# Kernel tuning notes

Hardware: AMD Instinct MI355X
Metric: run time of the kernel (lower is better)

Reference implementation:

```python
import jax, jax.numpy as jnp
import numpy as np

DEPTH = 2
DIM = 512
HEADS = 8
DH = 64
INNER = HEADS * DH
MLP = 2048
B = 2
N = 2048
EPS = 1e-6
NEG = -float(np.finfo(np.float32).max)
SCALE = DH ** -0.5


def setup_inputs() -> dict:
    key = jax.random.key(0)
    ks = jax.random.split(key, 8)
    inp = {
        'x': jax.random.normal(ks[0], (B, N, DIM), dtype=jnp.float32),
        'mask': jax.random.randint(ks[1], (B, N), 0, 2, dtype=jnp.int32),
        'qkv_w': 0.02 * jax.random.normal(ks[2], (DEPTH, DIM, 3 * INNER), dtype=jnp.float32),
        'out_w': 0.02 * jax.random.normal(ks[3], (DEPTH, INNER, DIM), dtype=jnp.float32),
        'out_b': jnp.zeros((DEPTH, DIM), dtype=jnp.float32),
        'ff_w1': 0.02 * jax.random.normal(ks[4], (DEPTH, DIM, MLP), dtype=jnp.float32),
        'ff_b1': jnp.zeros((DEPTH, MLP), dtype=jnp.float32),
        'ff_w2': 0.02 * jax.random.normal(ks[5], (DEPTH, MLP, DIM), dtype=jnp.float32),
        'ff_b2': jnp.zeros((DEPTH, DIM), dtype=jnp.float32),
        'ad1_w': jnp.ones((DEPTH, B * DIM), dtype=jnp.float32),
        'ad1_b': jnp.zeros((DEPTH, B * DIM), dtype=jnp.float32),
        'ad2_w': jnp.ones((DEPTH, B * DIM), dtype=jnp.float32),
        'ad2_b': jnp.zeros((DEPTH, B * DIM), dtype=jnp.float32),
    }
    return inp


def adain(x, w, b):
    # AdaptiveInstanceNorm2d: batch_norm over channels (B*D), spatial dim N, training=True
    # -> per-(b, d) mean/biased-var over N, affine params of shape (B*D,) -> (B,1,D)
    mu = jnp.mean(x, axis=1, keepdims=True)
    var = jnp.var(x, axis=1, keepdims=True)  # biased variance, as in batch_norm
    xn = (x - mu) * jax.lax.rsqrt(var + EPS)
    b_sz, _, d = x.shape
    return xn * w.reshape(b_sz, 1, d) + b.reshape(b_sz, 1, d)


def attention(x, mask2d, qkv_w, out_w, out_b):
    b_sz, n, _ = x.shape
    qkv = x @ qkv_w  # [B,N,3*INNER]
    q, k, v = jnp.split(qkv, 3, axis=-1)

    def split_heads(t):
        return t.reshape(b_sz, n, HEADS, DH).transpose(0, 2, 1, 3)  # [B,H,N,D]

    q, k, v = split_heads(q), split_heads(k), split_heads(v)
    dots = jnp.einsum('bhnd,bhmd->bhnm', q, k) * SCALE  # [B,H,N,N]
    dots = jnp.where(mask2d[:, None] == 0, NEG, dots)
    attn = jax.nn.softmax(dots, axis=-1)
    out = jnp.einsum('bhnm,bhmd->bhnd', attn, v)
    out = out.transpose(0, 2, 1, 3).reshape(b_sz, n, INNER)
    return out @ out_w + out_b


def feedforward(x, w1, b1, w2, b2):
    h = jax.nn.gelu(x @ w1 + b1, approximate=False)  # torch nn.GELU default = exact erf
    return h @ w2 + b2


def reference(x, mask, qkv_w, out_w, out_b, ff_w1, ff_b1, ff_w2, ff_b2,
              ad1_w, ad1_b, ad2_w, ad2_b):
    mask2d = mask[:, :, None] * mask[:, None, :]  # [B,N,N]
    for l in range(DEPTH):
        h = adain(x, ad1_w[l], ad1_b[l])
        x = attention(h, mask2d, qkv_w[l], out_w[l], out_b[l]) + x
        h = adain(x, ad2_w[l], ad2_b[l])
        x = feedforward(h, ff_w1[l], ff_b1[l], ff_w2[l], ff_b2[l]) + x
    return x
```

## Files before the change

### kernel.cpp

```cpp
#include <hip/hip_runtime.h>
#include <hip/hip_bf16.h>

#define DEPTHL 2
#define DIMM   512
#define NHEADS 8
#define DHH    64
#define INNERD 512
#define MLPD   2048
#define BB     2
#define SEQL   2048
#define ROWS   (BB*SEQL)
#define MNEG   (-1.0e38f)
#define SCLQ   0.18033688f
#define NSPLIT 4
#define KPS    (SEQL / NSPLIT)

typedef __attribute__((ext_vector_type(4))) float f32x4;
typedef __attribute__((ext_vector_type(8))) __bf16 bf16x8;

#define GLDS16(g, l) __builtin_amdgcn_global_load_lds((const __attribute__((address_space(1))) void*)(g), (__attribute__((address_space(3))) void*)(l), 16, 0, 0)

__device__ __forceinline__ unsigned short f2bf(float f) {
  union { float f; unsigned int u; } v; v.f = f;
  unsigned int r = v.u + 0x7fffu + ((v.u >> 16) & 1u);
  return (unsigned short)(r >> 16);
}
__device__ __forceinline__ float bf2f(unsigned short h) {
  union { unsigned int u; float f; } v; v.u = ((unsigned int)h) << 16; return v.f;
}
__device__ __forceinline__ unsigned int cvtpk(float a, float b) {
  unsigned int r;
  asm("v_cvt_pk_bf16_f32 %0, %1, %2" : "=v"(r) : "v"(a), "v"(b));
  return r;
}

__global__ __launch_bounds__(256) void wtrans(const float* __restrict__ wsrc,
                                              unsigned short* __restrict__ wdst,
                                              int K, int N) {
  __shared__ float t[32][33];
  const float* src = wsrc + (size_t)blockIdx.z * K * N;
  unsigned short* dst = wdst + (size_t)blockIdx.z * K * N;
  int k0 = blockIdx.x * 32, n0 = blockIdx.y * 32;
  int tx = threadIdx.x & 31, ty = threadIdx.x >> 5;
#pragma unroll
  for (int j = 0; j < 32; j += 8)
    t[ty + j][tx] = src[(size_t)(k0 + ty + j) * N + n0 + tx];
  __syncthreads();
#pragma unroll
  for (int j = 0; j < 32; j += 8)
    dst[(size_t)(n0 + ty + j) * K + k0 + tx] = f2bf(t[tx][ty + j]);
}

__global__ __launch_bounds__(512) void adain_p1(const float* __restrict__ x,
                                                float* __restrict__ p1, float* __restrict__ p2) {
  int d = threadIdx.x, c = blockIdx.x, b = blockIdx.y;
  const float* xp = x + ((size_t)b * SEQL + c * 64) * DIMM + d;
  float s = 0.f, s2 = 0.f;
  for (int i = 0; i < 64; ++i) { float v = xp[(size_t)i * DIMM]; s += v; s2 += v * v; }
  p1[(b * 32 + c) * DIMM + d] = s;
  p2[(b * 32 + c) * DIMM + d] = s2;
}

__global__ __launch_bounds__(512) void adain_p2(const float* __restrict__ p1, const float* __restrict__ p2,
                                                const float* __restrict__ w, const float* __restrict__ bi,
                                                float* __restrict__ alpha, float* __restrict__ beta) {
  int d = threadIdx.x, b = blockIdx.x;
  float s = 0.f, s2 = 0.f;
  for (int c = 0; c < 32; ++c) { s += p1[(b * 32 + c) * DIMM + d]; s2 += p2[(b * 32 + c) * DIMM + d]; }
  float mean = s * (1.0f / SEQL);
  float var = s2 * (1.0f / SEQL) - mean * mean;
  float a = w[b * DIMM + d] * rsqrtf(var + 1e-6f);
  alpha[b * DIMM + d] = a;
  beta[b * DIMM + d] = bi[b * DIMM + d] - mean * a;
}

__global__ __launch_bounds__(256) void adain_apply(const float* __restrict__ x,
                                                   const float* __restrict__ alpha, const float* __restrict__ beta,
                                                   unsigned short* __restrict__ hb) {
  int idx = blockIdx.x * 256 + threadIdx.x;
  int d = idx & (DIMM - 1);
  int b = idx >> 20;
  hb[idx] = f2bf(x[idx] * alpha[b * DIMM + d] + beta[b * DIMM + d]);
}

__global__ __launch_bounds__(256) void maskbuild(const int* __restrict__ mask, float* __restrict__ maskadd) {
  int i = blockIdx.x * 256 + threadIdx.x;
  maskadd[i] = mask[i] ? 0.f : MNEG;
}

template <int EPI, int BN>
__global__ __launch_bounds__(256)
void gemm_k(const unsigned short* __restrict__ A,
            const unsigned short* __restrict__ Wt,
            const float* __restrict__ bias,
            const float* __restrict__ resid,
            float* __restrict__ outF,
            unsigned short* __restrict__ outB,
            unsigned short* __restrict__ part,
            int N, int Kt) {
  constexpr int NI = BN / 32;
  __shared__ __align__(16) unsigned short As[2][128 * 32];
  __shared__ __align__(16) unsigned short Bs[2][BN * 32];
  const int tid = threadIdx.x;
  const int w = tid >> 6, lane = tid & 63;

  unsigned int f = blockIdx.y * gridDim.x + blockIdx.x;
  unsigned int grp = f & 7u, idx = f >> 3;
  unsigned int rpx = gridDim.y >> 3;
  unsigned int by = grp * rpx + idx / gridDim.x;
  unsigned int bx = idx % gridDim.x;

  const int bm = by * 128, bn = bx * BN;
  const int wm = (w >> 1) * 64, wn = (w & 1) * (BN / 2);

  const int nsplit = gridDim.z, sp = blockIdx.z;
  const int Kc = Kt / nsplit;
  const int kbeg = sp * Kc, kend = kbeg + Kc;

  f32x4 acc[4][NI] = {};

  auto stage = [&](int buf, int k0) {
#pragma unroll
    for (int j = 0; j < 2; ++j) {
      int r = w * 32 + (lane >> 2) + j * 16;
      int cl = (lane & 3) ^ ((r >> 1) & 3);
      GLDS16(A + (size_t)(bm + r) * Kt + k0 + cl * 8, &As[buf][(w * 32 + j * 16) * 32]);
    }
    if (BN == 128) {
#pragma unroll
      for (int j = 0; j < 2; ++j) {
        int r = w * 32 + (lane >> 2) + j * 16;
        int cl = (lane & 3) ^ ((r >> 1) & 3);
        GLDS16(Wt + (size_t)(bn + r) * Kt + k0 + cl * 8, &Bs[buf][(w * 32 + j * 16) * 32]);
      }
    } else {
      int r = w * 16 + (lane >> 2);
      int cl = (lane & 3) ^ ((r >> 1) & 3);
      GLDS16(Wt + (size_t)(bn + r) * Kt + k0 + cl * 8, &Bs[buf][(w * 16) * 32]);
    }
  };

  stage(0, kbeg);
  __syncthreads();
  int cur = 0;

  for (int k0 = kbeg; k0 < kend; k0 += 32) {
    if (k0 + 32 < kend) stage(cur ^ 1, k0 + 32);
    bf16x8 af[4], bfr[NI];
#pragma unroll
    for (int i = 0; i < 4; ++i) {
      int ar = wm + i * 16 + (lane & 15);
      int ac = (lane >> 4) ^ ((ar >> 1) & 3);
      af[i] = *(const bf16x8*)&As[cur][ar * 32 + ac * 8];
    }
#pragma unroll
    for (int i = 0; i < NI; ++i) {
      int br = wn + i * 16 + (lane & 15);
      int bc = (lane >> 4) ^ ((br >> 1) & 3);
      bfr[i] = *(const bf16x8*)&Bs[cur][br * 32 + bc * 8];
    }
#pragma unroll
    for (int mi = 0; mi < 4; ++mi)
#pragma unroll
      for (int ni = 0; ni < NI; ++ni)
        acc[mi][ni] = __builtin_amdgcn_mfma_f32_16x16x32_bf16(af[mi], bfr[ni], acc[mi][ni], 0, 0, 0);
    __syncthreads();
    cur ^= 1;
  }

  const size_t MN = (size_t)gridDim.y * 128 * N;
#pragma unroll
  for (int mi = 0; mi < 4; ++mi) {
#pragma unroll
    for (int ni = 0; ni < NI; ++ni) {
#pragma unroll
      for (int r = 0; r < 4; ++r) {
        int row = bm + wm + mi * 16 + (lane >> 4) * 4 + r;
        int col = bn + wn + ni * 16 + (lane & 15);
        float v = acc[mi][ni][r];
        size_t o = (size_t)row * N + col;
        if (EPI == 3) {
          part[(size_t)sp * MN + o] = f2bf(v);
        } else {
          if (bias) v += bias[col];
          if (EPI == 1) v = 0.5f * v * (1.0f + erff(v * 0.70710678118f));
          if (EPI == 2) outF[o] = v + resid[o];
          else if (EPI != 2) outB[o] = f2bf(v);
        }
      }
    }
  }
}

template <int NS>
__global__ __launch_bounds__(256) void comb_k(const unsigned short* __restrict__ part,
                                              const float* __restrict__ bias,
                                              const float* __restrict__ resid,
                                              float* __restrict__ outF) {
  size_t idx = ((size_t)blockIdx.x * 256 + threadIdx.x) * 4;
  int col = (int)(idx & 511);
  float a0 = 0.f, a1 = 0.f, a2 = 0.f, a3 = 0.f;
#pragma unroll
  for (int s = 0; s < NS; ++s) {
    uint2 v = *(const uint2*)&part[(size_t)s * ROWS * 512 + idx];
    a0 += bf2f(v.x & 0xffff); a1 += bf2f(v.x >> 16);
    a2 += bf2f(v.y & 0xffff); a3 += bf2f(v.y >> 16);
  }
  f32x4 b = *(const f32x4*)&bias[col];
  f32x4 rs = *(const f32x4*)&resid[idx];
  f32x4 o;
  o[0] = a0 + b[0] + rs[0]; o[1] = a1 + b[1] + rs[1];
  o[2] = a2 + b[2] + rs[2]; o[3] = a3 + b[3] + rs[3];
  *(f32x4*)&outF[idx] = o;
}

__global__ __launch_bounds__(256) void repack_qk(const unsigned short* __restrict__ qkv,
                                                 unsigned short* __restrict__ q,
                                                 unsigned short* __restrict__ k) {
  int idx = blockIdx.x * 256 + threadIdx.x;
  int d = idx & (INNERD - 1);
  int n = (idx >> 9) & (SEQL - 1);
  int b = idx >> 20;
  int h = d >> 6, dh = d & 63;
  size_t src = (size_t)(b * SEQL + n) * 1536 + d;
  size_t dst = ((size_t)(b * NHEADS + h) * SEQL + n) * DHH + dh;
  q[dst] = f2bf(bf2f(qkv[src]) * SCLQ);
  k[dst] = qkv[src + INNERD];
}

__global__ __launch_bounds__(256) void transpose_v(const unsigned short* __restrict__ qkv,
                                                   unsigned short* __restrict__ vt) {
  __shared__ unsigned short t[64][65];
  int bh = blockIdx.x;
  int nt = blockIdx.y;
  int b = bh >> 3, h = bh & 7;
  for (int i = threadIdx.x; i < 64 * 64; i += 256) {
    int n = i >> 6, dh = i & 63;
    t[n][dh] = qkv[(size_t)(b * SEQL + nt * 64 + n) * 1536 + 2 * INNERD + h * 64 + dh];
  }
  __syncthreads();
  for (int i = threadIdx.x; i < 64 * 64; i += 256) {
    int dh = i >> 6, n = i & 63;
    vt[((size_t)bh * DHH + dh) * SEQL + nt * 64 + n] = t[n][dh];
  }
}

__global__ __launch_bounds__(256) void vmean_k(const unsigned short* __restrict__ vt,
                                               float* __restrict__ vmean) {
  __shared__ float red[256];
  int bh = blockIdx.x, t = threadIdx.x;
  int d = blockIdx.y * 8 + (t >> 5), seg = t & 31;
  const unsigned short* p = vt + ((size_t)bh * 64 + d) * SEQL + seg * 64;
  float s = 0.f;
#pragma unroll
  for (int i = 0; i < 16; ++i) {
    uint2 v = *(const uint2*)&p[i * 4];
    s += bf2f(v.x & 0xffff) + bf2f(v.x >> 16) + bf2f(v.y & 0xffff) + bf2f(v.y >> 16);
  }
  red[t] = s;
  __syncthreads();
  if (t < 8) {
    float a = 0.f;
#pragma unroll
    for (int i = 0; i < 32; ++i) a += red[t * 32 + i];
    vmean[bh * 64 + blockIdx.y * 8 + t] = a * (1.0f / SEQL);
  }
}

__global__ __launch_bounds__(256, 4)
void attn_split(const unsigned short* __restrict__ qg,
                const unsigned short* __restrict__ kg,
                const unsigned short* __restrict__ vtg,
                const float* __restrict__ maskadd,
                unsigned short* __restrict__ opart,
                float* __restrict__ lpart) {
  __shared__ __align__(16) unsigned short Ks[64 * 64];
  __shared__ __align__(16) unsigned short Vts[64 * 64];
  __shared__ __align__(16) unsigned short Ps[4 * 16 * 64];
  const int tid = threadIdx.x, w = tid >> 6, lane = tid & 63;
  const int g = lane >> 4, c = lane & 15;
  const int bh = blockIdx.y, b = bh >> 3;
  const int qt = blockIdx.x;
  const int split = blockIdx.z;
  const int kv0 = split * KPS;
  const int q0 = qt * 64 + w * 16;
  const float* maskb = maskadd + b * SEQL;

  bf16x8 qf[2];
#pragma unroll
  for (int kb = 0; kb < 2; ++kb)
    qf[kb] = *(const bf16x8*)&qg[((size_t)bh * SEQL + q0 + c) * DHH + kb * 32 + g * 8];

  const __bf16 one1 = (__bf16)1.0f;
  const bf16x8 ones = {one1, one1, one1, one1, one1, one1, one1, one1};

  f32x4 o[4] = {};
  f32x4 lones = {};
  unsigned short* myP = &Ps[w * 1024];

  for (int kt = 0; kt < KPS / 64; ++kt) {
#pragma unroll
    for (int j = 0; j < 2; ++j) {
      int r = w * 16 + j * 8 + (lane >> 3);
      int cl = (lane & 7) ^ (r & 7);
      GLDS16(kg + ((size_t)bh * SEQL + kv0 + kt * 64 + r) * DHH + cl * 8, &Ks[(w * 16 + j * 8) * 64]);
      GLDS16(vtg + ((size_t)bh * DHH + r) * SEQL + kv0 + kt * 64 + cl * 8, &Vts[(w * 16 + j * 8) * 64]);
    }
    __syncthreads();

    f32x4 sT[4];
#pragma unroll
    for (int nt = 0; nt < 4; ++nt)
      sT[nt] = *(const f32x4*)&maskb[kv0 + kt * 64 + nt * 16 + g * 4];
#pragma unroll
    for (int nt = 0; nt < 4; ++nt) {
#pragma unroll
      for (int kb = 0; kb < 2; ++kb) {
        int kr = nt * 16 + c;
        int cs = (kb * 4 + g) ^ (kr & 7);
        bf16x8 kf = *(const bf16x8*)&Ks[kr * 64 + cs * 8];
        sT[nt] = __builtin_amdgcn_mfma_f32_16x16x32_bf16(kf, qf[kb], sT[nt], 0, 0, 0);
      }
    }

#pragma unroll
    for (int nt = 0; nt < 4; ++nt) {
      float pv0 = exp2f(sT[nt][0]), pv1 = exp2f(sT[nt][1]);
      float pv2 = exp2f(sT[nt][2]), pv3 = exp2f(sT[nt][3]);
      unsigned int lo = cvtpk(pv0, pv1), hi = cvtpk(pv2, pv3);
      int off = c * 64 + (((nt * 2 + (g >> 1)) ^ (c & 7)) << 3) + ((g & 1) << 2);
      *(uint2*)(myP + off) = make_uint2(lo, hi);
    }

#pragma unroll
    for (int kb = 0; kb < 2; ++kb) {
      bf16x8 pf = *(const bf16x8*)&myP[c * 64 + (((kb * 4 + g) ^ (c & 7)) << 3)];
      lones = __builtin_amdgcn_mfma_f32_16x16x32_bf16(pf, ones, lones, 0, 0, 0);
#pragma unroll
      for (int ni = 0; ni < 4; ++ni) {
        int vr = ni * 16 + c;
        int vc = (kb * 4 + g) ^ (vr & 7);
        bf16x8 vf = *(const bf16x8*)&Vts[vr * 64 + vc * 8];
        o[ni] = __builtin_amdgcn_mfma_f32_16x16x32_bf16(pf, vf, o[ni], 0, 0, 0);
      }
    }
    __syncthreads();
  }

  const size_t pb = ((size_t)split * 16 + bh) * SEQL;
#pragma unroll
  for (int ni = 0; ni < 4; ++ni)
#pragma unroll
    for (int r = 0; r < 4; ++r)
      opart[(pb + q0 + g * 4 + r) * DHH + ni * 16 + c] = f2bf(o[ni][r]);
  if (c == 0) {
#pragma unroll
    for (int r = 0; r < 4; ++r) lpart[pb + q0 + g * 4 + r] = lones[r];
  }
}

__global__ __launch_bounds__(256) void attn_combine(const unsigned short* __restrict__ opart,
                                                    const float* __restrict__ lpart,
                                                    const float* __restrict__ maskadd,
                                                    const float* __restrict__ vmean,
                                                    unsigned short* __restrict__ ctx) {
  int idx = blockIdx.x * 256 + threadIdx.x;
  int dq = idx & 15;
  int q = (idx >> 4) & (SEQL - 1);
  int bh = idx >> 15;
  int d0 = dq * 4;
  int b = bh >> 3, h = bh & 7;
  float o0 = 0.f, o1 = 0.f, o2 = 0.f, o3 = 0.f, L = 0.f;
#pragma unroll
  for (int s = 0; s < NSPLIT; ++s) {
    size_t base = ((size_t)s * 16 + bh) * SEQL + q;
    L += lpart[base];
    uint2 v = *(const uint2*)&opart[base * DHH + d0];
    o0 += bf2f(v.x & 0xffff); o1 += bf2f(v.x >> 16);
    o2 += bf2f(v.y & 0xffff); o3 += bf2f(v.y >> 16);
  }
  float r = 1.0f / L;
  o0 *= r; o1 *= r; o2 *= r; o3 *= r;
  if (maskadd[b * SEQL + q] != 0.f) {
    f32x4 vm = *(const f32x4*)&vmean[bh * 64 + d0];
    o0 = vm[0]; o1 = vm[1]; o2 = vm[2]; o3 = vm[3];
  }
  *(uint2*)&ctx[((size_t)(b * SEQL + q)) * INNERD + h * 64 + d0] =
      make_uint2(cvtpk(o0, o1), cvtpk(o2, o3));
}

extern "C" void kernel_launch(void* const* d_in, const int* in_sizes, int n_in,
                              void* d_out, int out_size, void* d_ws, size_t ws_size,
                              hipStream_t stream) {
  (void)in_sizes; (void)n_in; (void)out_size;
  const float* x_in = (const float*)d_in[0];
  const int* mask = (const int*)d_in[1];
  const float* qkv_w = (const float*)d_in[2];
  const float* out_w = (const float*)d_in[3];
  const float* out_b = (const float*)d_in[4];
  const float* ff_w1 = (const float*)d_in[5];
  const float* ff_b1 = (const float*)d_in[6];
  const float* ff_w2 = (const float*)d_in[7];
  const float* ff_b2 = (const float*)d_in[8];
  const float* ad1w = (const float*)d_in[9];
  const float* ad1b = (const float*)d_in[10];
  const float* ad2w = (const float*)d_in[11];
  const float* ad2b = (const float*)d_in[12];

  char* ws = (char*)d_ws;
  size_t off = 0;
  auto alloc = [&](size_t bytes) {
    char* p = ws + off;
    off = (off + bytes + 255) & ~(size_t)255;
    return p;
  };
  unsigned short* wtQ = (unsigned short*)alloc((size_t)DEPTHL * 1536 * 512 * 2);
  unsigned short* wtO = (unsigned short*)alloc((size_t)DEPTHL * 512 * 512 * 2);
  unsigned short* wtF1 = (unsigned short*)alloc((size_t)DEPTHL * 2048 * 512 * 2);
  unsigned short* wtF2 = (unsigned short*)alloc((size_t)DEPTHL * 512 * 2048 * 2);
  float* xc = (float*)alloc((size_t)ROWS * DIMM * 4);
  unsigned short* hbf = (unsigned short*)alloc((size_t)ROWS * DIMM * 2);
  unsigned short* qkvbf = (unsigned short*)alloc((size_t)ROWS * 1536 * 2);
  char* region2 = alloc((size_t)4 * 16 * SEQL * DHH * 2);
  unsigned short* qb = (unsigned short*)region2;
  unsigned short* kb = qb + (size_t)16 * SEQL * DHH;
  unsigned short* vtb = kb + (size_t)16 * SEQL * DHH;
  unsigned short* ctxb = vtb + (size_t)16 * SEQL * DHH;
  unsigned short* h1bf = (unsigned short*)region2;
  float* p1 = (float*)alloc((size_t)BB * 32 * DIMM * 4);
  float* p2 = (float*)alloc((size_t)BB * 32 * DIMM * 4);
  float* alpha = (float*)alloc((size_t)BB * DIMM * 4);
  float* beta = (float*)alloc((size_t)BB * DIMM * 4);
  float* maskadd = (float*)alloc((size_t)BB * SEQL * 4);
  unsigned short* opart = (unsigned short*)alloc((size_t)NSPLIT * 16 * SEQL * DHH * 2);
  float* lpart = (float*)alloc((size_t)NSPLIT * 16 * SEQL * 4);
  float* vmean = (float*)alloc((size_t)16 * 64 * 4);
  unsigned short* part = (unsigned short*)alloc((size_t)4 * ROWS * 512 * 2);
  const bool fits = off <= ws_size;

  hipMemcpyAsync(xc, x_in, (size_t)ROWS * DIMM * 4, hipMemcpyDeviceToDevice, stream);

  wtrans<<<dim3(512 / 32, 1536 / 32, DEPTHL), 256, 0, stream>>>(qkv_w, wtQ, 512, 1536);
  wtrans<<<dim3(512 / 32, 512 / 32, DEPTHL), 256, 0, stream>>>(out_w, wtO, 512, 512);
  wtrans<<<dim3(512 / 32, 2048 / 32, DEPTHL), 256, 0, stream>>>(ff_w1, wtF1, 512, 2048);
  wtrans<<<dim3(2048 / 32, 512 / 32, DEPTHL), 256, 0, stream>>>(ff_w2, wtF2, 2048, 512);
  maskbuild<<<BB * SEQL / 256, 256, 0, stream>>>(mask, maskadd);

  for (int l = 0; l < DEPTHL; ++l) {
    adain_p1<<<dim3(32, BB), 512, 0, stream>>>(xc, p1, p2);
    adain_p2<<<BB, 512, 0, stream>>>(p1, p2, ad1w + l * BB * DIMM, ad1b + l * BB * DIMM, alpha, beta);
    adain_apply<<<8192, 256, 0, stream>>>(xc, alpha, beta, hbf);
    gemm_k<0, 64><<<dim3(1536 / 64, ROWS / 128), 256, 0, stream>>>(
        hbf, wtQ + (size_t)l * 1536 * 512, nullptr, nullptr, nullptr, qkvbf, nullptr, 1536, 512);
    repack_qk<<<8192, 256, 0, stream>>>(qkvbf, qb, kb);
    transpose_v<<<dim3(16, 32), 256, 0, stream>>>(qkvbf, vtb);
    vmean_k<<<dim3(16, 8), 256, 0, stream>>>(vtb, vmean);
    attn_split<<<dim3(SEQL / 64, 16, NSPLIT), 256, 0, stream>>>(qb, kb, vtb, maskadd, opart, lpart);
    attn_combine<<<16 * SEQL * 16 / 256, 256, 0, stream>>>(opart, lpart, maskadd, vmean, ctxb);
    if (fits) {
      gemm_k<3, 64><<<dim3(512 / 64, ROWS / 128, 2), 256, 0, stream>>>(
          ctxb, wtO + (size_t)l * 512 * 512, nullptr, nullptr, nullptr, nullptr, part, 512, 512);
      comb_k<2><<<ROWS * 512 / 1024, 256, 0, stream>>>(part, out_b + l * DIMM, xc, xc);
    } else {
      gemm_k<2, 64><<<dim3(512 / 64, ROWS / 128), 256, 0, stream>>>(
          ctxb, wtO + (size_t)l * 512 * 512, out_b + l * DIMM, xc, xc, nullptr, nullptr, 512, 512);
    }
    adain_p1<<<dim3(32, BB), 512, 0, stream>>>(xc, p1, p2);
    adain_p2<<<BB, 512, 0, stream>>>(p1, p2, ad2w + l * BB * DIMM, ad2b + l * BB * DIMM, alpha, beta);
    adain_apply<<<8192, 256, 0, stream>>>(xc, alpha, beta, hbf);
    gemm_k<1, 64><<<dim3(2048 / 64, ROWS / 128), 256, 0, stream>>>(
        hbf, wtF1 + (size_t)l * 2048 * 512, ff_b1 + l * MLPD, nullptr, nullptr, h1bf, nullptr, 2048, 512);
    float* xout = (l == DEPTHL - 1) ? (float*)d_out : xc;
    if (fits) {
      gemm_k<3, 64><<<dim3(512 / 64, ROWS / 128, 4), 256, 0, stream>>>(
          h1bf, wtF2 + (size_t)l * 512 * 2048, nullptr, nullptr, nullptr, nullptr, part, 512, 2048);
      comb_k<4><<<ROWS * 512 / 1024, 256, 0, stream>>>(part, ff_b2 + l * DIMM, xc, xout);
    } else {
      gemm_k<2, 64><<<dim3(512 / 64, ROWS / 128), 256, 0, stream>>>(
          h1bf, wtF2 + (size_t)l * 512 * 2048, ff_b2 + l * DIMM, xc, xout, nullptr, nullptr, 512, 2048);
    }
  }
}
```

Measured before the change: 329.0 us.

## Fuse Q/K repack, V transpose and V-mean; double-buffer attention K/V tiles

Replaces the separate repack_qk, transpose_v and vmean_k kernels with one qkv_prep kernel that uses vectorized 16-byte loads and stores, and accumulates the V column sums with atomics into a buffer that is zeroed by a memset before each use. The attention kernel now double-buffers its K and V shared-memory tiles, issuing the next tile's async loads before computing on the current one, so load latency can overlap MFMA work. The AdaIN partial-sum pass is split into 128 chunks instead of 32 to spread the reduction over more blocks. The trade-offs are extra LDS use in attention, which may lower occupancy, an added memset launch, and atomic adds whose ordering makes the V sums non-deterministic in float.

```diff
diff --git a/kernel.cpp b/kernel.cpp
--- a/kernel.cpp
+++ b/kernel.cpp
@@ -14,6 +14,7 @@
 #define SCLQ   0.18033688f
 #define NSPLIT 4
 #define KPS    (SEQL / NSPLIT)
+#define NCH    128
 
 typedef __attribute__((ext_vector_type(4))) float f32x4;
 typedef __attribute__((ext_vector_type(8))) __bf16 bf16x8;
@@ -54,11 +55,12 @@
 __global__ __launch_bounds__(512) void adain_p1(const float* __restrict__ x,
                                                 float* __restrict__ p1, float* __restrict__ p2) {
   int d = threadIdx.x, c = blockIdx.x, b = blockIdx.y;
-  const float* xp = x + ((size_t)b * SEQL + c * 64) * DIMM + d;
+  const float* xp = x + ((size_t)b * SEQL + c * 16) * DIMM + d;
   float s = 0.f, s2 = 0.f;
-  for (int i = 0; i < 64; ++i) { float v = xp[(size_t)i * DIMM]; s += v; s2 += v * v; }
-  p1[(b * 32 + c) * DIMM + d] = s;
-  p2[(b * 32 + c) * DIMM + d] = s2;
+#pragma unroll
+  for (int i = 0; i < 16; ++i) { float v = xp[(size_t)i * DIMM]; s += v; s2 += v * v; }
+  p1[(b * NCH + c) * DIMM + d] = s;
+  p2[(b * NCH + c) * DIMM + d] = s2;
 }
 
 __global__ __launch_bounds__(512) void adain_p2(const float* __restrict__ p1, const float* __restrict__ p2,
@@ -66,7 +68,7 @@
                                                 float* __restrict__ alpha, float* __restrict__ beta) {
   int d = threadIdx.x, b = blockIdx.x;
   float s = 0.f, s2 = 0.f;
-  for (int c = 0; c < 32; ++c) { s += p1[(b * 32 + c) * DIMM + d]; s2 += p2[(b * 32 + c) * DIMM + d]; }
+  for (int c = 0; c < NCH; ++c) { s += p1[(b * NCH + c) * DIMM + d]; s2 += p2[(b * NCH + c) * DIMM + d]; }
   float mean = s * (1.0f / SEQL);
   float var = s2 * (1.0f / SEQL) - mean * mean;
   float a = w[b * DIMM + d] * rsqrtf(var + 1e-6f);
@@ -214,57 +216,51 @@
   *(f32x4*)&outF[idx] = o;
 }
 
-__global__ __launch_bounds__(256) void repack_qk(const unsigned short* __restrict__ qkv,
-                                                 unsigned short* __restrict__ q,
-                                                 unsigned short* __restrict__ k) {
-  int idx = blockIdx.x * 256 + threadIdx.x;
-  int d = idx & (INNERD - 1);
-  int n = (idx >> 9) & (SEQL - 1);
-  int b = idx >> 20;
-  int h = d >> 6, dh = d & 63;
-  size_t src = (size_t)(b * SEQL + n) * 1536 + d;
-  size_t dst = ((size_t)(b * NHEADS + h) * SEQL + n) * DHH + dh;
-  q[dst] = f2bf(bf2f(qkv[src]) * SCLQ);
-  k[dst] = qkv[src + INNERD];
-}
-
-__global__ __launch_bounds__(256) void transpose_v(const unsigned short* __restrict__ qkv,
-                                                   unsigned short* __restrict__ vt) {
+__global__ __launch_bounds__(256) void qkv_prep(const unsigned short* __restrict__ qkv,
+                                                unsigned short* __restrict__ q,
+                                                unsigned short* __restrict__ k,
+                                                unsigned short* __restrict__ vt,
+                                                float* __restrict__ vsum) {
   __shared__ unsigned short t[64][65];
-  int bh = blockIdx.x;
-  int nt = blockIdx.y;
-  int b = bh >> 3, h = bh & 7;
-  for (int i = threadIdx.x; i < 64 * 64; i += 256) {
-    int n = i >> 6, dh = i & 63;
-    t[n][dh] = qkv[(size_t)(b * SEQL + nt * 64 + n) * 1536 + 2 * INNERD + h * 64 + dh];
+  const int bh = blockIdx.x, nt = blockIdx.y;
+  const int b = bh >> 3, h = bh & 7;
+  const int n0 = nt * 64;
+  const int tid = threadIdx.x;
+  const int nloc = tid >> 3, dh0 = (tid & 7) * 8;
+#pragma unroll
+  for (int j = 0; j < 2; ++j) {
+    int n = nloc + j * 32;
+    size_t src = (size_t)(b * SEQL + n0 + n) * 1536 + h * 64 + dh0;
+    size_t dst = ((size_t)bh * SEQL + n0 + n) * 64 + dh0;
+    uint4 qv = *(const uint4*)&qkv[src];
+    uint4 qs;
+    qs.x = cvtpk(bf2f(qv.x & 0xffff) * SCLQ, bf2f(qv.x >> 16) * SCLQ);
+    qs.y = cvtpk(bf2f(qv.y & 0xffff) * SCLQ, bf2f(qv.y >> 16) * SCLQ);
+    qs.z = cvtpk(bf2f(qv.z & 0xffff) * SCLQ, bf2f(qv.z >> 16) * SCLQ);
+    qs.w = cvtpk(bf2f(qv.w & 0xffff) * SCLQ, bf2f(qv.w >> 16) * SCLQ);
+    *(uint4*)&q[dst] = qs;
+    *(uint4*)&k[dst] = *(const uint4*)&qkv[src + INNERD];
+    uint4 vv = *(const uint4*)&qkv[src + 2 * INNERD];
+    unsigned short* tr = &t[n][dh0];
+    tr[0] = (unsigned short)(vv.x & 0xffff); tr[1] = (unsigned short)(vv.x >> 16);
+    tr[2] = (unsigned short)(vv.y & 0xffff); tr[3] = (unsigned short)(vv.y >> 16);
+    tr[4] = (unsigned short)(vv.z & 0xffff); tr[5] = (unsigned short)(vv.z >> 16);
+    tr[6] = (unsigned short)(vv.w & 0xffff); tr[7] = (unsigned short)(vv.w >> 16);
   }
   __syncthreads();
-  for (int i = threadIdx.x; i < 64 * 64; i += 256) {
+#pragma unroll
+  for (int j = 0; j < 16; ++j) {
+    int i = tid + j * 256;
     int dh = i >> 6, n = i & 63;
-    vt[((size_t)bh * DHH + dh) * SEQL + nt * 64 + n] = t[n][dh];
-  }
-}
-
-__global__ __launch_bounds__(256) void vmean_k(const unsigned short* __restrict__ vt,
-                                               float* __restrict__ vmean) {
-  __shared__ float red[256];
-  int bh = blockIdx.x, t = threadIdx.x;
-  int d = blockIdx.y * 8 + (t >> 5), seg = t & 31;
-  const unsigned short* p = vt + ((size_t)bh * 64 + d) * SEQL + seg * 64;
+    vt[((size_t)bh * DHH + dh) * SEQL + n0 + n] = t[n][dh];
+  }
+  int dh = tid >> 2, seg = tid & 3;
   float s = 0.f;
 #pragma unroll
-  for (int i = 0; i < 16; ++i) {
-    uint2 v = *(const uint2*)&p[i * 4];
-    s += bf2f(v.x & 0xffff) + bf2f(v.x >> 16) + bf2f(v.y & 0xffff) + bf2f(v.y >> 16);
-  }
-  red[t] = s;
-  __syncthreads();
-  if (t < 8) {
-    float a = 0.f;
-#pragma unroll
-    for (int i = 0; i < 32; ++i) a += red[t * 32 + i];
-    vmean[bh * 64 + blockIdx.y * 8 + t] = a * (1.0f / SEQL);
-  }
+  for (int i = 0; i < 16; ++i) s += bf2f(t[seg * 16 + i][dh]);
+  s += __shfl_xor(s, 1);
+  s += __shfl_xor(s, 2);
+  if (seg == 0) atomicAdd(&vsum[bh * 64 + dh], s);
 }
 
 __global__ __launch_bounds__(256, 4)
@@ -274,8 +270,8 @@
                 const float* __restrict__ maskadd,
                 unsigned short* __restrict__ opart,
                 float* __restrict__ lpart) {
-  __shared__ __align__(16) unsigned short Ks[64 * 64];
-  __shared__ __align__(16) unsigned short Vts[64 * 64];
+  __shared__ __align__(16) unsigned short Ks[2][64 * 64];
+  __shared__ __align__(16) unsigned short Vts[2][64 * 64];
   __shared__ __align__(16) unsigned short Ps[4 * 16 * 64];
   const int tid = threadIdx.x, w = tid >> 6, lane = tid & 63;
   const int g = lane >> 4, c = lane & 15;
@@ -298,15 +294,22 @@
   f32x4 lones = {};
   unsigned short* myP = &Ps[w * 1024];
 
-  for (int kt = 0; kt < KPS / 64; ++kt) {
+  auto stageA = [&](int buf, int kt) {
 #pragma unroll
     for (int j = 0; j < 2; ++j) {
       int r = w * 16 + j * 8 + (lane >> 3);
       int cl = (lane & 7) ^ (r & 7);
-      GLDS16(kg + ((size_t)bh * SEQL + kv0 + kt * 64 + r) * DHH + cl * 8, &Ks[(w * 16 + j * 8) * 64]);
-      GLDS16(vtg + ((size_t)bh * DHH + r) * SEQL + kv0 + kt * 64 + cl * 8, &Vts[(w * 16 + j * 8) * 64]);
-    }
-    __syncthreads();
+      GLDS16(kg + ((size_t)bh * SEQL + kv0 + kt * 64 + r) * DHH + cl * 8, &Ks[buf][(w * 16 + j * 8) * 64]);
+      GLDS16(vtg + ((size_t)bh * DHH + r) * SEQL + kv0 + kt * 64 + cl * 8, &Vts[buf][(w * 16 + j * 8) * 64]);
+    }
+  };
+
+  stageA(0, 0);
+  __syncthreads();
+  int cur = 0;
+
+  for (int kt = 0; kt < KPS / 64; ++kt) {
+    if (kt + 1 < KPS / 64) stageA(cur ^ 1, kt + 1);
 
     f32x4 sT[4];
 #pragma unroll
@@ -318,7 +321,7 @@
       for (int kb = 0; kb < 2; ++kb) {
         int kr = nt * 16 + c;
         int cs = (kb * 4 + g) ^ (kr & 7);
-        bf16x8 kf = *(const bf16x8*)&Ks[kr * 64 + cs * 8];
+        bf16x8 kf = *(const bf16x8*)&Ks[cur][kr * 64 + cs * 8];
         sT[nt] = __builtin_amdgcn_mfma_f32_16x16x32_bf16(kf, qf[kb], sT[nt], 0, 0, 0);
       }
     }
@@ -340,11 +343,12 @@
       for (int ni = 0; ni < 4; ++ni) {
         int vr = ni * 16 + c;
         int vc = (kb * 4 + g) ^ (vr & 7);
-        bf16x8 vf = *(const bf16x8*)&Vts[vr * 64 + vc * 8];
+        bf16x8 vf = *(const bf16x8*)&Vts[cur][vr * 64 + vc * 8];
         o[ni] = __builtin_amdgcn_mfma_f32_16x16x32_bf16(pf, vf, o[ni], 0, 0, 0);
       }
     }
     __syncthreads();
+    cur ^= 1;
   }
 
   const size_t pb = ((size_t)split * 16 + bh) * SEQL;
@@ -362,7 +366,7 @@
 __global__ __launch_bounds__(256) void attn_combine(const unsigned short* __restrict__ opart,
                                                     const float* __restrict__ lpart,
                                                     const float* __restrict__ maskadd,
-                                                    const float* __restrict__ vmean,
+                                                    const float* __restrict__ vsum,
                                                     unsigned short* __restrict__ ctx) {
   int idx = blockIdx.x * 256 + threadIdx.x;
   int dq = idx & 15;
@@ -382,8 +386,9 @@
   float r = 1.0f / L;
   o0 *= r; o1 *= r; o2 *= r; o3 *= r;
   if (maskadd[b * SEQL + q] != 0.f) {
-    f32x4 vm = *(const f32x4*)&vmean[bh * 64 + d0];
-    o0 = vm[0]; o1 = vm[1]; o2 = vm[2]; o3 = vm[3];
+    f32x4 vm = *(const f32x4*)&vsum[bh * 64 + d0];
+    o0 = vm[0] * (1.0f / SEQL); o1 = vm[1] * (1.0f / SEQL);
+    o2 = vm[2] * (1.0f / SEQL); o3 = vm[3] * (1.0f / SEQL);
   }
   *(uint2*)&ctx[((size_t)(b * SEQL + q)) * INNERD + h * 64 + d0] =
       make_uint2(cvtpk(o0, o1), cvtpk(o2, o3));
@@ -427,14 +432,14 @@
   unsigned short* vtb = kb + (size_t)16 * SEQL * DHH;
   unsigned short* ctxb = vtb + (size_t)16 * SEQL * DHH;
   unsigned short* h1bf = (unsigned short*)region2;
-  float* p1 = (float*)alloc((size_t)BB * 32 * DIMM * 4);
-  float* p2 = (float*)alloc((size_t)BB * 32 * DIMM * 4);
+  float* p1 = (float*)alloc((size_t)BB * NCH * DIMM * 4);
+  float* p2 = (float*)alloc((size_t)BB * NCH * DIMM * 4);
   float* alpha = (float*)alloc((size_t)BB * DIMM * 4);
   float* beta = (float*)alloc((size_t)BB * DIMM * 4);
   float* maskadd = (float*)alloc((size_t)BB * SEQL * 4);
   unsigned short* opart = (unsigned short*)alloc((size_t)NSPLIT * 16 * SEQL * DHH * 2);
   float* lpart = (float*)alloc((size_t)NSPLIT * 16 * SEQL * 4);
-  float* vmean = (float*)alloc((size_t)16 * 64 * 4);
+  float* vsum = (float*)alloc((size_t)16 * 64 * 4);
   unsigned short* part = (unsigned short*)alloc((size_t)4 * ROWS * 512 * 2);
   const bool fits = off <= ws_size;
 
@@ -447,16 +452,15 @@
   maskbuild<<<BB * SEQL / 256, 256, 0, stream>>>(mask, maskadd);
 
   for (int l = 0; l < DEPTHL; ++l) {
-    adain_p1<<<dim3(32, BB), 512, 0, stream>>>(xc, p1, p2);
+    adain_p1<<<dim3(NCH, BB), 512, 0, stream>>>(xc, p1, p2);
     adain_p2<<<BB, 512, 0, stream>>>(p1, p2, ad1w + l * BB * DIMM, ad1b + l * BB * DIMM, alpha, beta);
     adain_apply<<<8192, 256, 0, stream>>>(xc, alpha, beta, hbf);
     gemm_k<0, 64><<<dim3(1536 / 64, ROWS / 128), 256, 0, stream>>>(
         hbf, wtQ + (size_t)l * 1536 * 512, nullptr, nullptr, nullptr, qkvbf, nullptr, 1536, 512);
-    repack_qk<<<8192, 256, 0, stream>>>(qkvbf, qb, kb);
-    transpose_v<<<dim3(16, 32), 256, 0, stream>>>(qkvbf, vtb);
-    vmean_k<<<dim3(16, 8), 256, 0, stream>>>(vtb, vmean);
+    hipMemsetAsync(vsum, 0, 16 * 64 * 4, stream);
+    qkv_prep<<<dim3(16, 32), 256, 0, stream>>>(qkvbf, qb, kb, vtb, vsum);
     attn_split<<<dim3(SEQL / 64, 16, NSPLIT), 256, 0, stream>>>(qb, kb, vtb, maskadd, opart, lpart);
-    attn_combine<<<16 * SEQL * 16 / 256, 256, 0, stream>>>(opart, lpart, maskadd, vmean, ctxb);
+    attn_combine<<<16 * SEQL * 16 / 256, 256, 0, stream>>>(opart, lpart, maskadd, vsum, ctxb);
     if (fits) {
       gemm_k<3, 64><<<dim3(512 / 64, ROWS / 128, 2), 256, 0, stream>>>(
           ctxb, wtO + (size_t)l * 512 * 512, nullptr, nullptr, nullptr, nullptr, part, 512, 512);
@@ -465,7 +469,7 @@
       gemm_k<2, 64><<<dim3(512 / 64, ROWS / 128), 256, 0, stream>>>(
           ctxb, wtO + (size_t)l * 512 * 512, out_b + l * DIMM, xc, xc, nullptr, nullptr, 512, 512);
     }
-    adain_p1<<<dim3(32, BB), 512, 0, stream>>>(xc, p1, p2);
+    adain_p1<<<dim3(NCH, BB), 512, 0, stream>>>(xc, p1, p2);
     adain_p2<<<BB, 512, 0, stream>>>(p1, p2, ad2w + l * BB * DIMM, ad2b + l * BB * DIMM, alpha, beta);
     adain_apply<<<8192, 256, 0, stream>>>(xc, alpha, beta, hbf);
     gemm_k<1, 64><<<dim3(2048 / 64, ROWS / 128), 256, 0, stream>>>(
```

New measurement: 337.2 us. 2.5% more time.
